# Optimization experiments

Measured on AMD Instinct MI355X. Metric: run time of the kernel, lower is better.

## Reference

```python
import jax, jax.numpy as jnp
import numpy as np

N, D = 8192, 256
NUM_CLASSES = 64


def setup_inputs() -> dict:
    key = jax.random.key(0)
    k1, k2 = jax.random.split(key)
    represent = jax.random.normal(k1, (N, D), dtype=jnp.float32)
    label = jax.random.randint(k2, (N,), 0, NUM_CLASSES, dtype=jnp.int64)
    t = jnp.float32(0.1)  # temperature
    return {"represent": represent, "label": label, "t": t}


def reference(represent, label, t):
    x = represent.astype(jnp.float32)                      # [N, D]
    norms = jnp.sqrt(jnp.sum(x * x, axis=-1))              # [N]
    # pairwise cosine: (x x^T) / (||xi|| ||xj||)
    cos = (x @ x.T) / (norms[:, None] * norms[None, :])    # [N, N]
    pos_mask = label[:, None] == label[None, :]            # [N, N] bool
    e = jnp.exp(cos / t)                                   # [N, N]
    # original computes exp(mask * cos / t): masked-out entries become exp(0) = 1
    pos_pair = jnp.where(pos_mask, e, 1.0).sum(axis=-1)    # [N]
    neg_pair = jnp.where(pos_mask, 1.0, e).sum(axis=-1)    # [N]
    loss = (jnp.log(neg_pair) - jnp.log(pos_pair)).sum() / represent.shape[0]
    return loss
```

## Files before the change

### kernel.cpp

```cpp
#include <hip/hip_runtime.h>

#define N_ROWS 8192
#define DIM 256
#define NUM_CLASSES 64
#define NBLK 64
#define NTRI (NBLK * (NBLK + 1) / 2)
#define SCR_PITCH 36

typedef float f32x4 __attribute__((ext_vector_type(4)));

__device__ __forceinline__ void gload_lds16(const void* g, void* l) {
  __builtin_amdgcn_global_load_lds(
      (const __attribute__((address_space(1))) unsigned int*)g,
      (__attribute__((address_space(3))) unsigned int*)l, 16, 0, 0);
}

__device__ __forceinline__ void tri_decode(int q, int& I, int& J) {
  int i = (int)((129.0f - sqrtf(16641.0f - 8.0f * (float)q)) * 0.5f);
  while (i * (129 - i) / 2 > q) --i;
  while ((i + 1) * (128 - i) / 2 <= q) ++i;
  I = i;
  J = i + (q - i * (129 - i) / 2);
}

__global__ void __launch_bounds__(256) prep_kernel(
    const float* __restrict__ x, const float* __restrict__ tptr,
    unsigned int* __restrict__ xq, float* __restrict__ sv,
    float* __restrict__ gsum, unsigned int* __restrict__ gcnt) {
  if (blockIdx.x == 0 && threadIdx.x == 0) { *gsum = 0.f; *gcnt = 0u; }
  const int row = blockIdx.x * 4 + (threadIdx.x >> 6);
  const int lane = threadIdx.x & 63;
  const float4 v = *reinterpret_cast<const float4*>(x + (size_t)row * DIM + lane * 4);
  int p = __builtin_amdgcn_cvt_pk_fp8_f32(v.x, v.y, 0, false);
  p = __builtin_amdgcn_cvt_pk_fp8_f32(v.z, v.w, p, true);
  const float f0 = __builtin_amdgcn_cvt_f32_fp8(p, 0);
  const float f1 = __builtin_amdgcn_cvt_f32_fp8(p, 1);
  const float f2 = __builtin_amdgcn_cvt_f32_fp8(p, 2);
  const float f3 = __builtin_amdgcn_cvt_f32_fp8(p, 3);
  float ss = f0 * f0 + f1 * f1 + f2 * f2 + f3 * f3;
  xq[(size_t)row * 64 + lane] = (unsigned int)p;
  for (int m = 32; m; m >>= 1) ss += __shfl_xor(ss, m, 64);
  if (lane == 0) sv[row] = sqrtf(1.4426950408889634f / tptr[0] / ss);
}

__global__ void __launch_bounds__(256, 3) main_kernel(
    const unsigned char* __restrict__ xb, const float* __restrict__ sv,
    const int* __restrict__ lab, float2* __restrict__ part) {
  const int q = blockIdx.x;
  int I, J;
  tri_decode(q, I, J);
  const int rowBase = I * 128;
  const int colBase = J * 128;

  __shared__ alignas(16) unsigned char buf[36864];
  __shared__ float colred[2][128][2];
  __shared__ float rsv[128]; __shared__ int rlab[128];
  __shared__ float csv[128]; __shared__ int clab[128];
  unsigned char* Al = buf;
  unsigned char* Bl = buf + 16384;
  float* scr0 = reinterpret_cast<float*>(buf);
  float* scr1 = reinterpret_cast<float*>(buf + 18432);

  const int tid = threadIdx.x;
  const int wave = tid >> 6;
  const int lane = tid & 63;
  const int quad = lane >> 4;
  const int lc = lane & 15;
  const int wrow = (wave >> 1) * 64;
  const int wcol = (wave & 1) * 64;
  const int ch = wave & 1;
  const int r8 = lane >> 3;
  const int c8 = lane & 7;

  if (tid < 128) {
    rsv[tid] = sv[rowBase + tid];
    rlab[tid] = lab[rowBase + tid];
    csv[tid] = sv[colBase + tid];
    clab[tid] = lab[colBase + tid];
  }

  const unsigned char* Ag = xb + (size_t)rowBase * DIM;
  const unsigned char* Bg = xb + (size_t)colBase * DIM;

#define STAGE_HALF(h)                                                         \
  {                                                                           \
    _Pragma("unroll") for (int i = 0; i < 4; ++i) {                           \
      const int r = wave * 32 + i * 8 + r8;                                   \
      const int gc = c8 ^ (r & 7);                                            \
      gload_lds16(Ag + (size_t)r * 256 + (h)*128 + gc * 16,                   \
                  Al + (wave * 32 + i * 8) * 128);                            \
      gload_lds16(Bg + (size_t)r * 256 + (h)*128 + gc * 16,                   \
                  Bl + (wave * 32 + i * 8) * 128);                            \
    }                                                                         \
  }

  f32x4 acc[4][4];
  const f32x4 zero4 = {0.f, 0.f, 0.f, 0.f};
  for (int mi = 0; mi < 4; ++mi)
    for (int ni = 0; ni < 4; ++ni) acc[mi][ni] = zero4;

  const int qh = quad >> 1, h8 = (quad & 1) * 8;
  int aOff[4], bOff[4];
#pragma unroll
  for (int mi = 0; mi < 4; ++mi)
    aOff[mi] = (wrow + mi * 16 + lc) * 128 + h8;
#pragma unroll
  for (int ni = 0; ni < 4; ++ni)
    bOff[ni] = (wcol + ni * 16 + lc) * 128 + h8;

  STAGE_HALF(0)
  __syncthreads();
#pragma unroll
  for (int half = 0; half < 2; ++half) {
#pragma unroll
    for (int kbl = 0; kbl < 4; ++kbl) {
      const int swz = (((kbl * 2 + qh) ^ (lc & 7)) << 4);
      long afr[4], bfr[4];
#pragma unroll
      for (int mi = 0; mi < 4; ++mi)
        afr[mi] = *reinterpret_cast<const long*>(Al + aOff[mi] + swz);
#pragma unroll
      for (int ni = 0; ni < 4; ++ni)
        bfr[ni] = *reinterpret_cast<const long*>(Bl + bOff[ni] + swz);
#pragma unroll
      for (int mi = 0; mi < 4; ++mi)
#pragma unroll
        for (int ni = 0; ni < 4; ++ni)
          acc[mi][ni] = __builtin_amdgcn_mfma_f32_16x16x32_fp8_fp8(
              afr[mi], bfr[ni], acc[mi][ni], 0, 0, 0);
    }
    __syncthreads();
    if (half == 0) {
      STAGE_HALF(1)
      __syncthreads();
    }
  }
#undef STAGE_HALF

  float scol[4];
  int labc[4];
#pragma unroll
  for (int ni = 0; ni < 4; ++ni) {
    scol[ni] = csv[wcol + ni * 16 + lc];
    labc[ni] = clab[wcol + ni * 16 + lc];
  }
  float ctot[4] = {0.f, 0.f, 0.f, 0.f};
  float csame[4] = {0.f, 0.f, 0.f, 0.f};

#pragma unroll
  for (int mi = 0; mi < 4; ++mi) {
#pragma unroll
    for (int r = 0; r < 4; ++r) {
      const int lr = wrow + mi * 16 + quad * 4 + r;
      const float siv = rsv[lr];
      const int li = rlab[lr];
      float st = 0.f, sm = 0.f;
#pragma unroll
      for (int ni = 0; ni < 4; ++ni) {
        const float e = exp2f(acc[mi][ni][r] * (siv * scol[ni]));
        const float em = (li == labc[ni]) ? e : 0.f;
        st += e;
        sm += em;
        ctot[ni] += e;
        csame[ni] += em;
      }
      scr0[lr * SCR_PITCH + ch * 16 + lc] = st;
      scr1[lr * SCR_PITCH + ch * 16 + lc] = sm;
    }
  }

  if (J > I) {
#pragma unroll
    for (int ni = 0; ni < 4; ++ni) {
      float t2 = ctot[ni] + __shfl_xor(ctot[ni], 16, 64);
      t2 += __shfl_xor(t2, 32, 64);
      float s2 = csame[ni] + __shfl_xor(csame[ni], 16, 64);
      s2 += __shfl_xor(s2, 32, 64);
      if (quad == 0) {
        colred[0][wcol + ni * 16 + lc][wave >> 1] = t2;
        colred[1][wcol + ni * 16 + lc][wave >> 1] = s2;
      }
    }
  }
  __syncthreads();

  if (tid < 128) {
    const int base = tid * SCR_PITCH;
    f32x4 a0 = {0.f, 0.f, 0.f, 0.f}, a1 = {0.f, 0.f, 0.f, 0.f};
#pragma unroll
    for (int k = 0; k < 8; ++k)
      a0 += *reinterpret_cast<const f32x4*>(&scr0[base + 4 * k]);
#pragma unroll
    for (int k = 0; k < 8; ++k)
      a1 += *reinterpret_cast<const f32x4*>(&scr1[base + 4 * k]);
    float2 v;
    v.x = a0[0] + a0[1] + a0[2] + a0[3];
    v.y = a1[0] + a1[1] + a1[2] + a1[3];
    part[(size_t)J * N_ROWS + rowBase + tid] = v;
    if (J > I) {
      float2 w;
      w.x = colred[0][tid][0] + colred[0][tid][1];
      w.y = colred[1][tid][0] + colred[1][tid][1];
      part[(size_t)I * N_ROWS + colBase + tid] = w;
    }
  }
}

__global__ void __launch_bounds__(256) row_loss_kernel(
    const float2* __restrict__ part, const int* __restrict__ lab,
    float* __restrict__ gsum, unsigned int* __restrict__ gcnt,
    float* __restrict__ out) {
  __shared__ int h[NUM_CLASSES];
  if (threadIdx.x < NUM_CLASSES) h[threadIdx.x] = 0;
  __syncthreads();
  for (int i = threadIdx.x; i < N_ROWS; i += 256) atomicAdd(&h[lab[i]], 1);
  __syncthreads();

  const int row = blockIdx.x * 256 + threadIdx.x;
  float st = 0.f, sm = 0.f;
#pragma unroll 8
  for (int b = 0; b < 64; ++b) {
    const float2 v = part[(size_t)b * N_ROWS + row];
    st += v.x;
    sm += v.y;
  }
  const int c = h[lab[row]];
  const float pos = sm + (float)(N_ROWS - c);
  const float neg = (st - sm) + (float)c;
  float term = logf(neg) - logf(pos);
  for (int m = 32; m; m >>= 1) term += __shfl_xor(term, m, 64);
  __shared__ float wsum[4];
  const int lane = threadIdx.x & 63;
  const int wave = threadIdx.x >> 6;
  if (lane == 0) wsum[wave] = term;
  __syncthreads();
  if (threadIdx.x == 0) {
    atomicAdd(gsum, wsum[0] + wsum[1] + wsum[2] + wsum[3]);
    __threadfence();
    const unsigned int t = atomicAdd(gcnt, 1u);
    if (t == (unsigned int)(N_ROWS / 256 - 1)) {
      const float total = atomicAdd(gsum, 0.0f);
      out[0] = total * (1.0f / (float)N_ROWS);
    }
  }
}

extern "C" void kernel_launch(void* const* d_in, const int* in_sizes, int n_in,
                              void* d_out, int out_size, void* d_ws, size_t ws_size,
                              hipStream_t stream) {
  const float* x = (const float*)d_in[0];
  const int* lab = (const int*)d_in[1];
  const float* t = (const float*)d_in[2];
  float* out = (float*)d_out;

  char* ws = (char*)d_ws;
  unsigned int* xq = (unsigned int*)ws;
  float* sv = (float*)(ws + (2u << 20));
  float2* part = (float2*)(ws + (2u << 20) + (32u << 10));
  float* gsum = (float*)(ws + (6u << 20) + (32u << 10));
  unsigned int* gcnt = (unsigned int*)(ws + (6u << 20) + (32u << 10) + 8);

  prep_kernel<<<N_ROWS / 4, 256, 0, stream>>>(x, t, xq, sv, gsum, gcnt);
  main_kernel<<<NTRI, 256, 0, stream>>>((const unsigned char*)xq, sv, lab, part);
  row_loss_kernel<<<N_ROWS / 256, 256, 0, stream>>>(part, lab, gsum, gcnt, out);
}
```

Baseline: 98.62 us.

## Fuse row-loss reduction into main kernel via per-rowblock arrival counters

Removes the third kernel launch by having the last tile block that finishes each 128-row block do the final per-row log-loss reduction, tracked with padded atomic arrival counters. The class histogram moves into prep_kernel as 32 partial histograms, so the finalizer no longer rescans all 8192 labels per block. This saves a launch and the tail of the reduction kernel, but adds atomics, fences and a serialized finalize step on whichever blocks arrive last.

```diff
diff --git a/kernel.cpp b/kernel.cpp
--- a/kernel.cpp
+++ b/kernel.cpp
@@ -24,12 +24,14 @@
 }
 
 __global__ void __launch_bounds__(256) prep_kernel(
-    const float* __restrict__ x, const float* __restrict__ tptr,
-    unsigned int* __restrict__ xq, float* __restrict__ sv,
-    float* __restrict__ gsum, unsigned int* __restrict__ gcnt) {
-  if (blockIdx.x == 0 && threadIdx.x == 0) { *gsum = 0.f; *gcnt = 0u; }
-  const int row = blockIdx.x * 4 + (threadIdx.x >> 6);
-  const int lane = threadIdx.x & 63;
+    const float* __restrict__ x, const int* __restrict__ lab,
+    const float* __restrict__ tptr, unsigned int* __restrict__ xq,
+    float* __restrict__ sv, int* __restrict__ hpart,
+    unsigned int* __restrict__ arrive, float* __restrict__ gsum,
+    unsigned int* __restrict__ gcnt) {
+  const int tid = threadIdx.x;
+  const int row = blockIdx.x * 4 + (tid >> 6);
+  const int lane = tid & 63;
   const float4 v = *reinterpret_cast<const float4*>(x + (size_t)row * DIM + lane * 4);
   int p = __builtin_amdgcn_cvt_pk_fp8_f32(v.x, v.y, 0, false);
   p = __builtin_amdgcn_cvt_pk_fp8_f32(v.z, v.w, p, true);
@@ -41,11 +43,68 @@
   xq[(size_t)row * 64 + lane] = (unsigned int)p;
   for (int m = 32; m; m >>= 1) ss += __shfl_xor(ss, m, 64);
   if (lane == 0) sv[row] = sqrtf(1.4426950408889634f / tptr[0] / ss);
+
+  if (blockIdx.x < 32) {
+    __shared__ int h[NUM_CLASSES];
+    if (tid < NUM_CLASSES) h[tid] = 0;
+    __syncthreads();
+    atomicAdd(&h[lab[blockIdx.x * 256 + tid]], 1);
+    __syncthreads();
+    if (tid < NUM_CLASSES) hpart[blockIdx.x * NUM_CLASSES + tid] = h[tid];
+  }
+  if (blockIdx.x == 0) {
+    for (int i = tid; i < NBLK * 16; i += 256) arrive[i] = 0u;
+    if (tid == 0) { *gsum = 0.f; *gcnt = 0u; }
+  }
+}
+
+__device__ __forceinline__ void finalize_rowblock(
+    int R, const float2* __restrict__ part, const int* __restrict__ lab,
+    const int* __restrict__ hpart, float* __restrict__ gsum,
+    unsigned int* __restrict__ gcnt, float* __restrict__ out, int tid,
+    int* cls, float* fred) {
+  if (tid < NUM_CLASSES) {
+    int s = 0;
+#pragma unroll
+    for (int k = 0; k < 32; ++k) s += hpart[k * NUM_CLASSES + tid];
+    cls[tid] = s;
+  }
+  __syncthreads();
+  float term = 0.f;
+  if (tid < 128) {
+    const int row = R * 128 + tid;
+    float st = 0.f, sm = 0.f;
+#pragma unroll 8
+    for (int b = 0; b < 64; ++b) {
+      const float2 v = part[(size_t)b * N_ROWS + row];
+      st += v.x;
+      sm += v.y;
+    }
+    const int c = cls[lab[row]];
+    const float pos = sm + (float)(N_ROWS - c);
+    const float neg = (st - sm) + (float)c;
+    term = logf(neg) - logf(pos);
+  }
+  for (int m = 32; m; m >>= 1) term += __shfl_xor(term, m, 64);
+  if (tid < 128 && (tid & 63) == 0) fred[tid >> 6] = term;
+  __syncthreads();
+  if (tid == 0) {
+    atomicAdd(gsum, fred[0] + fred[1]);
+    __threadfence();
+    const unsigned int t = atomicAdd(gcnt, 1u);
+    if (t == (unsigned int)(NBLK - 1)) {
+      out[0] = atomicAdd(gsum, 0.0f) * (1.0f / (float)N_ROWS);
+    }
+  }
+  __syncthreads();
 }
 
 __global__ void __launch_bounds__(256, 3) main_kernel(
     const unsigned char* __restrict__ xb, const float* __restrict__ sv,
-    const int* __restrict__ lab, float2* __restrict__ part) {
+    const int* __restrict__ lab, float2* __restrict__ part,
+    const int* __restrict__ hpart, unsigned int* __restrict__ arrive,
+    float* __restrict__ gsum, unsigned int* __restrict__ gcnt,
+    float* __restrict__ out) {
   const int q = blockIdx.x;
   int I, J;
   tri_decode(q, I, J);
@@ -56,6 +115,9 @@
   __shared__ float colred[2][128][2];
   __shared__ float rsv[128]; __shared__ int rlab[128];
   __shared__ float csv[128]; __shared__ int clab[128];
+  __shared__ int cls[NUM_CLASSES];
+  __shared__ float fred[2];
+  __shared__ int doneA, doneB;
   unsigned char* Al = buf;
   unsigned char* Bl = buf + 16384;
   float* scr0 = reinterpret_cast<float*>(buf);
@@ -204,45 +266,20 @@
       part[(size_t)I * N_ROWS + colBase + tid] = w;
     }
   }
-}
-
-__global__ void __launch_bounds__(256) row_loss_kernel(
-    const float2* __restrict__ part, const int* __restrict__ lab,
-    float* __restrict__ gsum, unsigned int* __restrict__ gcnt,
-    float* __restrict__ out) {
-  __shared__ int h[NUM_CLASSES];
-  if (threadIdx.x < NUM_CLASSES) h[threadIdx.x] = 0;
-  __syncthreads();
-  for (int i = threadIdx.x; i < N_ROWS; i += 256) atomicAdd(&h[lab[i]], 1);
-  __syncthreads();
-
-  const int row = blockIdx.x * 256 + threadIdx.x;
-  float st = 0.f, sm = 0.f;
-#pragma unroll 8
-  for (int b = 0; b < 64; ++b) {
-    const float2 v = part[(size_t)b * N_ROWS + row];
-    st += v.x;
-    sm += v.y;
-  }
-  const int c = h[lab[row]];
-  const float pos = sm + (float)(N_ROWS - c);
-  const float neg = (st - sm) + (float)c;
-  float term = logf(neg) - logf(pos);
-  for (int m = 32; m; m >>= 1) term += __shfl_xor(term, m, 64);
-  __shared__ float wsum[4];
-  const int lane = threadIdx.x & 63;
-  const int wave = threadIdx.x >> 6;
-  if (lane == 0) wsum[wave] = term;
-  __syncthreads();
-  if (threadIdx.x == 0) {
-    atomicAdd(gsum, wsum[0] + wsum[1] + wsum[2] + wsum[3]);
+  __syncthreads();
+
+  if (tid == 0) {
     __threadfence();
-    const unsigned int t = atomicAdd(gcnt, 1u);
-    if (t == (unsigned int)(N_ROWS / 256 - 1)) {
-      const float total = atomicAdd(gsum, 0.0f);
-      out[0] = total * (1.0f / (float)N_ROWS);
-    }
-  }
+    doneA = (atomicAdd(&arrive[I * 16], 1u) == (unsigned int)(NBLK - 1));
+    doneB = 0;
+    if (J > I)
+      doneB = (atomicAdd(&arrive[J * 16], 1u) == (unsigned int)(NBLK - 1));
+  }
+  __syncthreads();
+  if (doneA)
+    finalize_rowblock(I, part, lab, hpart, gsum, gcnt, out, tid, cls, fred);
+  if (doneB)
+    finalize_rowblock(J, part, lab, hpart, gsum, gcnt, out, tid, cls, fred);
 }
 
 extern "C" void kernel_launch(void* const* d_in, const int* in_sizes, int n_in,
@@ -259,8 +296,11 @@
   float2* part = (float2*)(ws + (2u << 20) + (32u << 10));
   float* gsum = (float*)(ws + (6u << 20) + (32u << 10));
   unsigned int* gcnt = (unsigned int*)(ws + (6u << 20) + (32u << 10) + 8);
-
-  prep_kernel<<<N_ROWS / 4, 256, 0, stream>>>(x, t, xq, sv, gsum, gcnt);
-  main_kernel<<<NTRI, 256, 0, stream>>>((const unsigned char*)xq, sv, lab, part);
-  row_loss_kernel<<<N_ROWS / 256, 256, 0, stream>>>(part, lab, gsum, gcnt, out);
-}
+  int* hpart = (int*)(ws + (6u << 20) + (33u << 10));
+  unsigned int* arrive = (unsigned int*)(ws + (6u << 20) + (42u << 10));
+
+  prep_kernel<<<N_ROWS / 4, 256, 0, stream>>>(x, lab, t, xq, sv, hpart, arrive,
+                                              gsum, gcnt);
+  main_kernel<<<NTRI, 256, 0, stream>>>((const unsigned char*)xq, sv, lab, part,
+                                        hpart, arrive, gsum, gcnt, out);
+}
```

Result: slower. 145.6 us (+47.6%).
